# Performance work log

Measured on AMD Instinct MI355X. Metric: run time of the kernel, lower is better.

Reference implementation:

```python
import jax, jax.numpy as jnp
import numpy as np

B, S, D, M, O = 16, 1024, 1024, 1024, 1024


def _sq_cdist(x1, x2):
    # squared euclidean distance, shapes (..., n, d) x (..., m, d) -> (..., n, m)
    n1 = jnp.sum(x1 * x1, axis=-1, keepdims=True)            # (..., n, 1)
    n2 = jnp.sum(x2 * x2, axis=-1)[..., None, :]             # (..., 1, m)
    cross = jnp.einsum('...nd,...md->...nm', x1, x2)
    return jnp.maximum(n1 + n2 - 2.0 * cross, 0.0)


def _rbf(x1, x2, log_lengthscale):
    ls2 = jnp.exp(log_lengthscale) ** 2
    return jnp.exp(-0.5 * _sq_cdist(x1, x2) / ls2)


def setup_inputs() -> dict:
    key = jax.random.key(0)
    k1, k2, k3 = jax.random.split(key, 3)
    x = jax.random.normal(k1, (B, S, D), dtype=jnp.float32)
    inducing_points = jax.random.normal(k2, (M, D), dtype=jnp.float32)
    log_lengthscale = jnp.zeros((1,), dtype=jnp.float32)
    log_noise = jnp.zeros((1,), dtype=jnp.float32)
    # nn.Linear(n_inducing, output_dim).weight has shape (O, M)
    lim = 1.0 / np.sqrt(M)
    W_out = jax.random.uniform(k3, (O, M), minval=-lim, maxval=lim, dtype=jnp.float32)
    return {
        'x': x,
        'inducing_points': inducing_points,
        'log_lengthscale': log_lengthscale,
        'log_noise': log_noise,
        'W_out': W_out,
        'num_sentences': S,
    }


def reference(x, inducing_points, log_lengthscale, log_noise, W_out, num_sentences):
    ll = log_lengthscale[0]
    K_xx = _rbf(x, x, ll)                                    # (B, S, S)
    K_xi = _rbf(x, inducing_points[None], ll)                # (B, S, M)
    K_ii = _rbf(inducing_points, inducing_points, ll)        # (M, M)
    K_ii_reg = K_ii + jnp.exp(log_noise[0]) * jnp.eye(M, dtype=x.dtype)
    K_ii_inv = jnp.linalg.inv(K_ii_reg)                      # (M, M)
    A = jnp.einsum('bsm,mk->bsk', K_xi, K_ii_inv)            # (B, S, M)
    mean = jnp.einsum('bsm,om->bso', A, W_out)               # (B, S, O)
    var = K_xx - jnp.einsum('bsm,btm->bst', A, K_xi)         # (B, S, S)
    var_diag = jnp.diagonal(var, axis1=-2, axis2=-1)         # (B, S)
    var_out = jnp.broadcast_to(var_diag[..., None], (x.shape[0], num_sentences, W_out.shape[0]))
    return mean, jax.nn.softplus(var_out)
```

## Files before the change

### kernel.cpp

```cpp
#include <hip/hip_runtime.h>
#include <hip/hip_bf16.h>
#include <math.h>


typedef unsigned short u16;
typedef __attribute__((ext_vector_type(8))) short short8;
typedef __attribute__((ext_vector_type(4))) float f32x4;
typedef __attribute__((ext_vector_type(4))) unsigned short us4;

__device__ __forceinline__ float bf2f(u16 b) {
  union { unsigned u; float f; } x; x.u = ((unsigned)b) << 16; return x.f;
}
__device__ __forceinline__ u16 f2bf(float f) {
  union { float f; unsigned u; } x; x.f = f;
  unsigned r = x.u + 0x7fffu + ((x.u >> 16) & 1u);
  return (u16)(r >> 16);
}

__device__ __forceinline__ void gl_lds16(const void* g, void* l) {
  __builtin_amdgcn_global_load_lds(
      (const __attribute__((address_space(1))) void*)g,
      (__attribute__((address_space(3))) void*)l, 16, 0, 0);
}

template <int EPI>
__global__ __launch_bounds__(512, 1) void gemm8(
    const u16* __restrict__ Ag, const u16* __restrict__ Bg,
    float* __restrict__ outF, float* __restrict__ varF,
    u16* __restrict__ outB,
    const float* __restrict__ rowN, const float* __restrict__ colN,
    const float* __restrict__ p_ll, float* __restrict__ qb) {
  __shared__ u16 lds[65536];
  constexpr int NT = 16;
  const int tid = threadIdx.x;
  const int lane = tid & 63;
  const int wave = tid >> 6;
  const int wr = wave >> 2, wc = wave & 3;
  const int fro = lane & 15, khi = lane >> 4;
  const int bid = blockIdx.x;
  const int xcd = bid & 7, j5 = bid >> 3;
  const size_t brow = (size_t)(xcd * 8 + (j5 >> 2));
  const size_t bcol = (size_t)(j5 & 3);

  if (EPI == 0) {
    if (tid < 64) qb[(size_t)bid * 64 + tid] = 0.0f;
  }

  const int c0 = tid, c1 = tid + 512;
  const int r0 = c0 >> 3, r1 = c1 >> 3;
  const int gk0 = (c0 & 7) ^ (r0 & 7), gk1 = (c1 & 7) ^ (r1 & 7);
  const int d0 = c0 * 8, d1 = c1 * 8;

  f32x4 acc[8][4] = {};

  auto stageA = [&](int tt, int h, int bb) {
    const u16* s0 = Ag + (size_t)(brow * 256 + h * 128 + r0) * 1024 + tt * 64 + gk0 * 8;
    const u16* s1 = Ag + (size_t)(brow * 256 + h * 128 + r1) * 1024 + tt * 64 + gk1 * 8;
    gl_lds16(s0, &lds[bb * 32768 + h * 8192 + d0]);
    gl_lds16(s1, &lds[bb * 32768 + h * 8192 + d1]);
  };
  auto stageB = [&](int tt, int h, int bb) {
    const u16* s0 = Bg + (size_t)(bcol * 256 + h * 128 + r0) * 1024 + tt * 64 + gk0 * 8;
    const u16* s1 = Bg + (size_t)(bcol * 256 + h * 128 + r1) * 1024 + tt * 64 + gk1 * 8;
    gl_lds16(s0, &lds[bb * 32768 + 16384 + h * 8192 + d0]);
    gl_lds16(s1, &lds[bb * 32768 + 16384 + h * 8192 + d1]);
  };

  stageA(0, 0, 0); stageA(0, 1, 0);
  stageB(0, 0, 0); stageB(0, 1, 0);
  stageB(1, 0, 1); stageB(1, 1, 1);
  stageA(1, 0, 1);
  asm volatile("s_waitcnt vmcnt(6)" ::: "memory");
  __builtin_amdgcn_s_barrier();

  for (int t = 0; t < NT; ++t) {
    const int cb = t & 1;
    const int abase = cb * 32768 + wr * 8192;
    const int bbase = cb * 32768 + 16384 + (wc >> 1) * 8192;
    short8 bfrag[4][2];
#pragma unroll
    for (int p = 0; p < 4; ++p) {
      short8 afr[2][2];
#pragma unroll
      for (int i = 0; i < 2; ++i) {
        const int rr = (p * 2 + i) * 16 + fro;
#pragma unroll
        for (int s = 0; s < 2; ++s) {
          const int kl = (s * 4 + khi) ^ (rr & 7);
          afr[i][s] = *(const short8*)&lds[abase + (rr * 8 + kl) * 8];
        }
      }
      if (p == 0) {
#pragma unroll
        for (int n = 0; n < 4; ++n) {
          const int cc = (wc & 1) * 64 + n * 16 + fro;
#pragma unroll
          for (int s = 0; s < 2; ++s) {
            const int kl = (s * 4 + khi) ^ (cc & 7);
            bfrag[n][s] = *(const short8*)&lds[bbase + (cc * 8 + kl) * 8];
          }
        }
      }
      if (p == 0) {
        if (t + 1 < NT) stageA(t + 1, 1, (t + 1) & 1);
      } else if (p == 1) {
        if (t + 2 < NT) stageB(t + 2, 0, cb);
      } else if (p == 2) {
        if (t + 2 < NT) {
          stageB(t + 2, 1, cb);
          stageA(t + 2, 0, cb);
        }
      }
      __builtin_amdgcn_s_barrier();
      __builtin_amdgcn_s_setprio(1);
#pragma unroll
      for (int i = 0; i < 2; ++i)
#pragma unroll
        for (int n = 0; n < 4; ++n)
#pragma unroll
          for (int s = 0; s < 2; ++s)
            acc[p * 2 + i][n] = __builtin_amdgcn_mfma_f32_16x16x32_bf16(
                afr[i][s], bfrag[n][s], acc[p * 2 + i][n], 0, 0, 0);
      __builtin_amdgcn_s_setprio(0);
      if (p == 3) {
        if (t < NT - 2) asm volatile("s_waitcnt vmcnt(6)" ::: "memory");
        else            asm volatile("s_waitcnt vmcnt(0)" ::: "memory");
      }
      __builtin_amdgcn_s_barrier();
    }
  }

  float inv2 = 0.f;
  if (EPI == 0) inv2 = 0.5f * expf(-2.0f * p_ll[0]);
#pragma unroll
  for (int m = 0; m < 8; m++) {
#pragma unroll
    for (int j = 0; j < 4; j++) {
      const size_t grow = brow * 256 + wr * 128 + m * 16 + khi * 4 + j;
      float rn = 0.f, sp = 0.f;
      if (EPI == 0) rn = rowN[grow];
      if (EPI == 1) {
        float vq = 1.0f - qb[grow];
        sp = fmaxf(vq, 0.f) + log1pf(expf(-fabsf(vq)));
      }
      float part = 0.f;
#pragma unroll
      for (int n = 0; n < 4; n++) {
        const size_t gcol = bcol * 256 + wc * 64 + n * 16 + fro;
        const size_t o = grow * 1024 + gcol;
        float v = acc[m][n][j];
        if (EPI == 0) {
          float d2 = fmaxf(rn + colN[gcol] - 2.0f * v, 0.0f);
          outB[o] = f2bf(expf(-inv2 * d2));
        } else if (EPI == 1) {
          outF[o] = v;
          varF[o] = sp;
        } else {
          part += v * v;
        }
      }
      if (EPI == 2) {
        part += __shfl_xor(part, 1);
        part += __shfl_xor(part, 2);
        part += __shfl_xor(part, 4);
        part += __shfl_xor(part, 8);
        if (fro == 0) atomicAdd(&qb[grow], part);
      }
    }
  }
}

__device__ __forceinline__ void small_core(const u16* __restrict__ Ap,
                                           const u16* __restrict__ Bp,
                                           u16* As, u16* Bs,
                                           f32x4 (&acc)[4][4]) {
  const int tid = threadIdx.x;
  const int lane = tid & 63;
  const int wave = tid >> 6;
  const int wr = wave >> 1, wc = wave & 1;
  const int idx0 = tid, idx1 = tid + 256;
  const u16* gA0 = Ap + (size_t)(idx0 >> 2) * 1024 + (size_t)(idx0 & 3) * 8;
  const u16* gA1 = Ap + (size_t)(idx1 >> 2) * 1024 + (size_t)(idx1 & 3) * 8;
  const u16* gB0 = Bp + (size_t)(idx0 >> 2) * 1024 + (size_t)(idx0 & 3) * 8;
  const u16* gB1 = Bp + (size_t)(idx1 >> 2) * 1024 + (size_t)(idx1 & 3) * 8;
  u16* lA0 = &As[idx0 * 8]; u16* lA1 = &As[idx1 * 8];
  u16* lB0 = &Bs[idx0 * 8]; u16* lB1 = &Bs[idx1 * 8];
  const int fro = lane & 15;
  const int ko = (lane >> 4) * 8;

  for (int kt = 0; kt < 1024; kt += 32) {
    gl_lds16(gA0 + kt, lA0);
    gl_lds16(gA1 + kt, lA1);
    gl_lds16(gB0 + kt, lB0);
    gl_lds16(gB1 + kt, lB1);
    __syncthreads();
    short8 af[4], bfr[4];
#pragma unroll
    for (int m = 0; m < 4; m++) {
      af[m]  = *(const short8*)&As[(wr * 64 + m * 16 + fro) * 32 + ko];
      bfr[m] = *(const short8*)&Bs[(wc * 64 + m * 16 + fro) * 32 + ko];
    }
#pragma unroll
    for (int m = 0; m < 4; m++)
#pragma unroll
      for (int n = 0; n < 4; n++)
        acc[m][n] = __builtin_amdgcn_mfma_f32_16x16x32_bf16(af[m], bfr[n], acc[m][n], 0, 0, 0);
    __syncthreads();
  }
}

__global__ __launch_bounds__(256) void gemm_kii(const u16* __restrict__ ipb,
                                                u16* __restrict__ kii,
                                                const float* __restrict__ ni,
                                                const float* __restrict__ ll,
                                                const float* __restrict__ ln,
                                                float* __restrict__ rs) {
  __shared__ u16 As[4096], Bs[4096];
  f32x4 acc[4][4] = {};
  small_core(ipb + (size_t)blockIdx.y * 131072, ipb + (size_t)blockIdx.x * 131072,
             As, Bs, acc);
  const int lane = threadIdx.x & 63;
  const int wave = threadIdx.x >> 6;
  const int wr = wave >> 1, wc = wave & 1;
  float inv2 = 0.5f * expf(-2.0f * ll[0]);
  float noise = expf(ln[0]);
#pragma unroll
  for (int m = 0; m < 4; m++)
#pragma unroll
    for (int j = 0; j < 4; j++) {
      const size_t grow = blockIdx.y * 128 + wr * 64 + m * 16 + (lane >> 4) * 4 + j;
      float rn = ni[grow];
      float part = 0.f;
#pragma unroll
      for (int n = 0; n < 4; n++) {
        const size_t gcol = blockIdx.x * 128 + wc * 64 + n * 16 + (lane & 15);
        float d2 = fmaxf(rn + ni[gcol] - 2.0f * acc[m][n][j], 0.0f);
        float kv = (grow == gcol) ? (1.0f + noise) : expf(-inv2 * d2);
        kii[grow * 1024 + gcol] = f2bf(kv);
        part += fabsf(kv);
      }
      part += __shfl_xor(part, 1);
      part += __shfl_xor(part, 2);
      part += __shfl_xor(part, 4);
      part += __shfl_xor(part, 8);
      if ((lane & 15) == 0) atomicAdd(&rs[grow], part);
    }
}

__global__ __launch_bounds__(256) void gemm_batch1(const u16* __restrict__ kii,
                                                   const u16* __restrict__ Wb,
                                                   u16* __restrict__ R2b,
                                                   u16* __restrict__ T1b,
                                                   const float* __restrict__ sc) {
  __shared__ u16 As[4096], Bs[4096];
  f32x4 acc[4][4] = {};
  const int z = blockIdx.z;
  const u16* Abase = z ? Wb : kii;
  small_core(Abase + (size_t)blockIdx.y * 131072, kii + (size_t)blockIdx.x * 131072,
             As, Bs, acc);
  const int lane = threadIdx.x & 63;
  const int wave = threadIdx.x >> 6;
  const int wr = wave >> 1, wc = wave & 1;
  const float c = sc[0];
#pragma unroll
  for (int m = 0; m < 4; m++)
#pragma unroll
    for (int j = 0; j < 4; j++) {
      const size_t grow = blockIdx.y * 128 + wr * 64 + m * 16 + (lane >> 4) * 4 + j;
#pragma unroll
      for (int n = 0; n < 4; n++) {
        const size_t gcol = blockIdx.x * 128 + wc * 64 + n * 16 + (lane & 15);
        const size_t o = grow * 1024 + gcol;
        float v = acc[m][n][j];
        if (z == 0) {
          float idv = (grow == gcol) ? 1.0f : 0.0f;
          R2b[o] = f2bf(idv - 2.0f * c * bf2f(kii[o]) + c * c * v);
        } else {
          T1b[o] = f2bf(2.0f * bf2f(Wb[o]) - c * v);
        }
      }
    }
}

__global__ __launch_bounds__(256) void gemm_batch2(const u16* __restrict__ kii,
                                                   const u16* __restrict__ R2b,
                                                   const u16* __restrict__ T1b,
                                                   u16* __restrict__ U,
                                                   const float* __restrict__ sc) {
  __shared__ u16 As[4096], Bs[4096];
  f32x4 acc[4][4] = {};
  const int z = blockIdx.z;
  const u16* Abase = z ? T1b : kii;
  small_core(Abase + (size_t)blockIdx.y * 131072, R2b + (size_t)blockIdx.x * 131072,
             As, Bs, acc);
  const int lane = threadIdx.x & 63;
  const int wave = threadIdx.x >> 6;
  const int wr = wave >> 1, wc = wave & 1;
  const float c = sc[0], s = sc[1];
#pragma unroll
  for (int m = 0; m < 4; m++)
#pragma unroll
    for (int j = 0; j < 4; j++) {
      const size_t grow = blockIdx.y * 128 + wr * 64 + m * 16 + (lane >> 4) * 4 + j;
#pragma unroll
      for (int n = 0; n < 4; n++) {
        const size_t gcol = blockIdx.x * 128 + wc * 64 + n * 16 + (lane & 15);
        const size_t o = grow * 1024 + gcol;
        float v = acc[m][n][j];
        if (z == 0) {
          float idv = (grow == gcol) ? 1.0f : 0.0f;
          U[o] = f2bf(s * (1.5f * idv - 0.5f * c * bf2f(kii[o]) +
                           0.6875f * bf2f(R2b[o]) - 0.3125f * c * v));
        } else {
          U[o + 1048576] = f2bf(c * (bf2f(T1b[o]) + v));
        }
      }
    }
}

__global__ __launch_bounds__(256) void prep_rows(const float* __restrict__ in,
                                                 u16* __restrict__ outb,
                                                 float* __restrict__ norms, int R) {
  __shared__ float wsum[4];
  for (int r = blockIdx.x; r < R; r += gridDim.x) {
    const float4 v = ((const float4*)(in + (size_t)r * 1024))[threadIdx.x];
    float ss = v.x * v.x + v.y * v.y + v.z * v.z + v.w * v.w;
    us4 o; o.x = f2bf(v.x); o.y = f2bf(v.y); o.z = f2bf(v.z); o.w = f2bf(v.w);
    ((us4*)(outb + (size_t)r * 1024))[threadIdx.x] = o;
#pragma unroll
    for (int s = 32; s > 0; s >>= 1) ss += __shfl_xor(ss, s);
    if ((threadIdx.x & 63) == 0) wsum[threadIdx.x >> 6] = ss;
    __syncthreads();
    if (threadIdx.x == 0) norms[r] = wsum[0] + wsum[1] + wsum[2] + wsum[3];
    __syncthreads();
  }
}

__global__ __launch_bounds__(256) void prep_ipw(const float* __restrict__ ip,
                                                const float* __restrict__ W,
                                                u16* __restrict__ ipb,
                                                u16* __restrict__ wbf,
                                                float* __restrict__ ni,
                                                float* __restrict__ rs) {
  __shared__ float wsum[4];
  int b = blockIdx.x;
  if (b < 1024) {
    const float4 v = ((const float4*)(ip + (size_t)b * 1024))[threadIdx.x];
    float ss = v.x * v.x + v.y * v.y + v.z * v.z + v.w * v.w;
    us4 o; o.x = f2bf(v.x); o.y = f2bf(v.y); o.z = f2bf(v.z); o.w = f2bf(v.w);
    ((us4*)(ipb + (size_t)b * 1024))[threadIdx.x] = o;
#pragma unroll
    for (int s = 32; s > 0; s >>= 1) ss += __shfl_xor(ss, s);
    if ((threadIdx.x & 63) == 0) wsum[threadIdx.x >> 6] = ss;
    __syncthreads();
    if (threadIdx.x == 0) {
      ni[b] = wsum[0] + wsum[1] + wsum[2] + wsum[3];
      rs[b] = 0.0f;
    }
  } else {
    int r = b - 1024;
    const float4 v = ((const float4*)(W + (size_t)r * 1024))[threadIdx.x];
    us4 o; o.x = f2bf(v.x); o.y = f2bf(v.y); o.z = f2bf(v.z); o.w = f2bf(v.w);
    ((us4*)(wbf + (size_t)r * 1024))[threadIdx.x] = o;
  }
}

__global__ __launch_bounds__(256) void gmax_inv(const float* __restrict__ rs,
                                                float* __restrict__ sc) {
  __shared__ float wm[4];
  float m = 0.f;
  for (int i = threadIdx.x; i < 1024; i += 256) m = fmaxf(m, rs[i]);
#pragma unroll
  for (int o = 32; o > 0; o >>= 1) m = fmaxf(m, __shfl_xor(m, o));
  if ((threadIdx.x & 63) == 0) wm[threadIdx.x >> 6] = m;
  __syncthreads();
  if (threadIdx.x == 0) {
    float c = 1.0f / fmaxf(fmaxf(wm[0], wm[1]), fmaxf(wm[2], wm[3]));
    sc[0] = c;
    sc[1] = sqrtf(c);
  }
}

extern "C" void kernel_launch(void* const* d_in, const int* in_sizes, int n_in,
                              void* d_out, int out_size, void* d_ws, size_t ws_size,
                              hipStream_t stream) {
  const float* x  = (const float*)d_in[0];
  const float* ip = (const float*)d_in[1];
  const float* ll = (const float*)d_in[2];
  const float* ln = (const float*)d_in[3];
  const float* W  = (const float*)d_in[4];

  char* ws = (char*)d_ws;
  const size_t MB = 1ull << 20;
  u16* kxib = (u16*)(ws + 0 * MB);
  u16* xbf  = (u16*)(ws + 32 * MB);
  u16* ipb  = (u16*)(ws + 64 * MB);
  u16* wbf  = (u16*)(ws + 66 * MB);
  u16* kii  = (u16*)(ws + 68 * MB);
  u16* R2b  = (u16*)(ws + 70 * MB);
  u16* Ub   = (u16*)(ws + 74 * MB);
  u16* t1b  = (u16*)(ws + 78 * MB);
  float* nx = (float*)(ws + 80 * MB);
  float* qb = (float*)(ws + 80 * MB + 128 * 1024);
  float* ni = (float*)(ws + 80 * MB + 256 * 1024);
  float* rs = (float*)(ws + 80 * MB + 512 * 1024);
  float* sc = (float*)(ws + 80 * MB + 768 * 1024);

  float* meanO = (float*)d_out;
  float* varO  = meanO + 16777216ull;

  prep_rows<<<2048, 256, 0, stream>>>(x, xbf, nx, 16384);
  prep_ipw<<<2048, 256, 0, stream>>>(ip, W, ipb, wbf, ni, rs);

  gemm_kii<<<dim3(8, 8), 256, 0, stream>>>(ipb, kii, ni, ll, ln, rs);
  gmax_inv<<<1, 256, 0, stream>>>(rs, sc);

  gemm_batch1<<<dim3(8, 8, 2), 256, 0, stream>>>(kii, wbf, R2b, t1b, sc);
  gemm_batch2<<<dim3(8, 8, 2), 256, 0, stream>>>(kii, R2b, t1b, Ub, sc);

  gemm8<0><<<256, 512, 0, stream>>>(xbf, ipb, nullptr, nullptr, kxib,
                                    nx, ni, ll, qb);
  gemm8<2><<<256, 512, 0, stream>>>(kxib, Ub, nullptr, nullptr, nullptr,
                                    nullptr, nullptr, nullptr, qb);
  gemm8<1><<<256, 512, 0, stream>>>(kxib, Ub + 1048576, meanO, varO, nullptr,
                                    nullptr, nullptr, nullptr, qb);
}
```

Before: 244.5 us.

## Replace 256x256 GEMM tiles with 128x128 tiles at two blocks per CU

The three main batched GEMMs move from 256x256 output tiles (512 threads, one block per CU) to 128x128 tiles with 256 threads and two blocks per CU. The launch grows from 256 to 1024 blocks. LDS staging, the prefetch schedule and the epilogue indexing are reworked to match, and one barrier per sub-step is removed. The goal is better occupancy, load balance and latency hiding across the 256 CUs, at the cost of less data reuse per tile and more global and L2 traffic.

```diff
diff --git a/kernel.cpp b/kernel.cpp
--- a/kernel.cpp
+++ b/kernel.cpp
@@ -24,106 +24,95 @@
 }
 
 template <int EPI>
-__global__ __launch_bounds__(512, 1) void gemm8(
+__global__ __launch_bounds__(256, 2) void gemm128(
     const u16* __restrict__ Ag, const u16* __restrict__ Bg,
     float* __restrict__ outF, float* __restrict__ varF,
     u16* __restrict__ outB,
     const float* __restrict__ rowN, const float* __restrict__ colN,
     const float* __restrict__ p_ll, float* __restrict__ qb) {
-  __shared__ u16 lds[65536];
+  __shared__ u16 lds[32768];
   constexpr int NT = 16;
   const int tid = threadIdx.x;
   const int lane = tid & 63;
   const int wave = tid >> 6;
-  const int wr = wave >> 2, wc = wave & 3;
+  const int wr = wave >> 1, wc = wave & 1;
   const int fro = lane & 15, khi = lane >> 4;
   const int bid = blockIdx.x;
-  const int xcd = bid & 7, j5 = bid >> 3;
-  const size_t brow = (size_t)(xcd * 8 + (j5 >> 2));
-  const size_t bcol = (size_t)(j5 & 3);
+  const int xcd = bid & 7, j7 = bid >> 3;
+  const size_t brow = (size_t)(xcd * 16 + (j7 >> 3));
+  const size_t bcol = (size_t)(j7 & 7);
 
   if (EPI == 0) {
-    if (tid < 64) qb[(size_t)bid * 64 + tid] = 0.0f;
-  }
-
-  const int c0 = tid, c1 = tid + 512;
-  const int r0 = c0 >> 3, r1 = c1 >> 3;
-  const int gk0 = (c0 & 7) ^ (r0 & 7), gk1 = (c1 & 7) ^ (r1 & 7);
-  const int d0 = c0 * 8, d1 = c1 * 8;
-
-  f32x4 acc[8][4] = {};
-
-  auto stageA = [&](int tt, int h, int bb) {
-    const u16* s0 = Ag + (size_t)(brow * 256 + h * 128 + r0) * 1024 + tt * 64 + gk0 * 8;
-    const u16* s1 = Ag + (size_t)(brow * 256 + h * 128 + r1) * 1024 + tt * 64 + gk1 * 8;
-    gl_lds16(s0, &lds[bb * 32768 + h * 8192 + d0]);
-    gl_lds16(s1, &lds[bb * 32768 + h * 8192 + d1]);
+    if (tid < 16) qb[(size_t)bid * 16 + tid] = 0.0f;
+  }
+
+  f32x4 acc[4][4] = {};
+
+  auto stageA = [&](int tt, int bb) {
+#pragma unroll
+    for (int c = 0; c < 4; ++c) {
+      const int ci = tid + 256 * c;
+      const int row = ci >> 3;
+      const int gk = (ci & 7) ^ (row & 7);
+      gl_lds16(Ag + (size_t)(brow * 128 + row) * 1024 + tt * 64 + gk * 8,
+               &lds[bb * 16384 + ci * 8]);
+    }
   };
-  auto stageB = [&](int tt, int h, int bb) {
-    const u16* s0 = Bg + (size_t)(bcol * 256 + h * 128 + r0) * 1024 + tt * 64 + gk0 * 8;
-    const u16* s1 = Bg + (size_t)(bcol * 256 + h * 128 + r1) * 1024 + tt * 64 + gk1 * 8;
-    gl_lds16(s0, &lds[bb * 32768 + 16384 + h * 8192 + d0]);
-    gl_lds16(s1, &lds[bb * 32768 + 16384 + h * 8192 + d1]);
+  auto stageB = [&](int tt, int bb) {
+#pragma unroll
+    for (int c = 0; c < 4; ++c) {
+      const int ci = tid + 256 * c;
+      const int row = ci >> 3;
+      const int gk = (ci & 7) ^ (row & 7);
+      gl_lds16(Bg + (size_t)(bcol * 128 + row) * 1024 + tt * 64 + gk * 8,
+               &lds[bb * 16384 + 8192 + ci * 8]);
+    }
   };
 
-  stageA(0, 0, 0); stageA(0, 1, 0);
-  stageB(0, 0, 0); stageB(0, 1, 0);
-  stageB(1, 0, 1); stageB(1, 1, 1);
-  stageA(1, 0, 1);
-  asm volatile("s_waitcnt vmcnt(6)" ::: "memory");
+  stageA(0, 0);
+  stageB(0, 0);
+  stageB(1, 1);
+  asm volatile("s_waitcnt vmcnt(4)" ::: "memory");
   __builtin_amdgcn_s_barrier();
 
   for (int t = 0; t < NT; ++t) {
     const int cb = t & 1;
-    const int abase = cb * 32768 + wr * 8192;
-    const int bbase = cb * 32768 + 16384 + (wc >> 1) * 8192;
+    const int ab = cb * 16384;
+    const int bb = cb * 16384 + 8192;
     short8 bfrag[4][2];
 #pragma unroll
     for (int p = 0; p < 4; ++p) {
-      short8 afr[2][2];
-#pragma unroll
-      for (int i = 0; i < 2; ++i) {
-        const int rr = (p * 2 + i) * 16 + fro;
-#pragma unroll
-        for (int s = 0; s < 2; ++s) {
-          const int kl = (s * 4 + khi) ^ (rr & 7);
-          afr[i][s] = *(const short8*)&lds[abase + (rr * 8 + kl) * 8];
-        }
+      short8 afr[2];
+      const int rr = wr * 64 + p * 16 + fro;
+#pragma unroll
+      for (int s = 0; s < 2; ++s) {
+        const int kl = (s * 4 + khi) ^ (rr & 7);
+        afr[s] = *(const short8*)&lds[ab + (rr * 8 + kl) * 8];
       }
       if (p == 0) {
 #pragma unroll
         for (int n = 0; n < 4; ++n) {
-          const int cc = (wc & 1) * 64 + n * 16 + fro;
+          const int cc = wc * 64 + n * 16 + fro;
 #pragma unroll
           for (int s = 0; s < 2; ++s) {
             const int kl = (s * 4 + khi) ^ (cc & 7);
-            bfrag[n][s] = *(const short8*)&lds[bbase + (cc * 8 + kl) * 8];
+            bfrag[n][s] = *(const short8*)&lds[bb + (cc * 8 + kl) * 8];
           }
         }
-      }
-      if (p == 0) {
-        if (t + 1 < NT) stageA(t + 1, 1, (t + 1) & 1);
+        if (t + 1 < NT) stageA(t + 1, cb ^ 1);
       } else if (p == 1) {
-        if (t + 2 < NT) stageB(t + 2, 0, cb);
-      } else if (p == 2) {
-        if (t + 2 < NT) {
-          stageB(t + 2, 1, cb);
-          stageA(t + 2, 0, cb);
-        }
-      }
-      __builtin_amdgcn_s_barrier();
+        if (t + 2 < NT) stageB(t + 2, cb);
+      }
       __builtin_amdgcn_s_setprio(1);
 #pragma unroll
-      for (int i = 0; i < 2; ++i)
-#pragma unroll
-        for (int n = 0; n < 4; ++n)
-#pragma unroll
-          for (int s = 0; s < 2; ++s)
-            acc[p * 2 + i][n] = __builtin_amdgcn_mfma_f32_16x16x32_bf16(
-                afr[i][s], bfrag[n][s], acc[p * 2 + i][n], 0, 0, 0);
+      for (int n = 0; n < 4; ++n)
+#pragma unroll
+        for (int s = 0; s < 2; ++s)
+          acc[p][n] = __builtin_amdgcn_mfma_f32_16x16x32_bf16(
+              afr[s], bfrag[n][s], acc[p][n], 0, 0, 0);
       __builtin_amdgcn_s_setprio(0);
       if (p == 3) {
-        if (t < NT - 2) asm volatile("s_waitcnt vmcnt(6)" ::: "memory");
+        if (t < NT - 2) asm volatile("s_waitcnt vmcnt(4)" ::: "memory");
         else            asm volatile("s_waitcnt vmcnt(0)" ::: "memory");
       }
       __builtin_amdgcn_s_barrier();
@@ -133,10 +122,10 @@
   float inv2 = 0.f;
   if (EPI == 0) inv2 = 0.5f * expf(-2.0f * p_ll[0]);
 #pragma unroll
-  for (int m = 0; m < 8; m++) {
+  for (int m = 0; m < 4; m++) {
 #pragma unroll
     for (int j = 0; j < 4; j++) {
-      const size_t grow = brow * 256 + wr * 128 + m * 16 + khi * 4 + j;
+      const size_t grow = brow * 128 + wr * 64 + m * 16 + khi * 4 + j;
       float rn = 0.f, sp = 0.f;
       if (EPI == 0) rn = rowN[grow];
       if (EPI == 1) {
@@ -146,7 +135,7 @@
       float part = 0.f;
 #pragma unroll
       for (int n = 0; n < 4; n++) {
-        const size_t gcol = bcol * 256 + wc * 64 + n * 16 + fro;
+        const size_t gcol = bcol * 128 + wc * 64 + n * 16 + fro;
         const size_t o = grow * 1024 + gcol;
         float v = acc[m][n][j];
         if (EPI == 0) {
@@ -418,10 +407,10 @@
   gemm_batch1<<<dim3(8, 8, 2), 256, 0, stream>>>(kii, wbf, R2b, t1b, sc);
   gemm_batch2<<<dim3(8, 8, 2), 256, 0, stream>>>(kii, R2b, t1b, Ub, sc);
 
-  gemm8<0><<<256, 512, 0, stream>>>(xbf, ipb, nullptr, nullptr, kxib,
-                                    nx, ni, ll, qb);
-  gemm8<2><<<256, 512, 0, stream>>>(kxib, Ub, nullptr, nullptr, nullptr,
-                                    nullptr, nullptr, nullptr, qb);
-  gemm8<1><<<256, 512, 0, stream>>>(kxib, Ub + 1048576, meanO, varO, nullptr,
-                                    nullptr, nullptr, nullptr, qb);
-}
+  gemm128<0><<<1024, 256, 0, stream>>>(xbf, ipb, nullptr, nullptr, kxib,
+                                       nx, ni, ll, qb);
+  gemm128<2><<<1024, 256, 0, stream>>>(kxib, Ub, nullptr, nullptr, nullptr,
+                                       nullptr, nullptr, nullptr, qb);
+  gemm128<1><<<1024, 256, 0, stream>>>(kxib, Ub + 1048576, meanO, varO, nullptr,
+                                       nullptr, nullptr, nullptr, qb);
+}
```

Measured after the change: 239.9 us. No clear change (-1.9%).
